# Kernel optimization log

Measured on AMD Instinct MI355X. Metric: run time of the kernel, lower is better.

Reference implementation:

```python
import jax, jax.numpy as jnp
import numpy as np

B, S = 16, 8192
D_MODEL = 128          # config.moe_intermediate_size
D_HID = 512            # config.intermediate_size
N_EXPERTS = 8
BEH_DIM = 32           # config.behavior_embedding_dim
N_BEH = 16             # config.num_behavior -> embedding rows = N_BEH + 1


def setup_inputs() -> dict:
    key = jax.random.key(0)
    k1, k2, k3, k4, k5, k6 = jax.random.split(key, 6)
    hidden_states = jax.random.normal(k1, (B, S, D_MODEL), dtype=jnp.float32)
    position_index = jax.random.randint(k2, (B, S), 0, N_EXPERTS, dtype=jnp.int32)
    behavior_index = jax.random.randint(k3, (B, S), 0, N_BEH + 1, dtype=jnp.int32)
    din = D_MODEL + BEH_DIM
    # expert weights: wi maps (D_MODEL+BEH_DIM)->D_HID, wo maps D_HID->D_MODEL (no bias)
    Wi = jax.random.normal(k4, (N_EXPERTS, din, D_HID), dtype=jnp.float32) * (din ** -0.5)
    Wo = jax.random.normal(k5, (N_EXPERTS, D_HID, D_MODEL), dtype=jnp.float32) * (D_HID ** -0.5)
    emb = jax.random.normal(k6, (N_BEH + 1, BEH_DIM), dtype=jnp.float32)
    return {"hidden_states": hidden_states, "position_index": position_index,
            "behavior_index": behavior_index, "Wi": Wi, "Wo": Wo, "emb": emb}


def reference(hidden_states, position_index, behavior_index, Wi, Wo, emb):
    # behavior injection: concat learned behavior embedding onto each token
    x = jnp.concatenate([hidden_states, emb[behavior_index]], axis=-1)  # [B,S,Din]
    out = jnp.zeros_like(hidden_states)
    # sparse expert dispatch: each token routed to exactly one expert by position_index
    # (loop over small fixed expert count; dropout is identity at p=0 / eval)
    for e in range(Wi.shape[0]):
        h = jax.nn.relu(jnp.einsum('bsd,dh->bsh', x, Wi[e]))   # [B,S,H]
        y = jnp.einsum('bsh,hd->bsd', h, Wo[e])                # [B,S,D]
        out = out + jnp.where((position_index == e)[..., None], y, 0.0)
    return out
```

## Files before the change

### kernel.cpp

```cpp
#include <hip/hip_runtime.h>
#include <stdint.h>

typedef short bf16x8 __attribute__((ext_vector_type(8)));
typedef float f32x4 __attribute__((ext_vector_type(4)));
typedef unsigned short ushort_t;
typedef ushort_t ushort8 __attribute__((ext_vector_type(8)));

#define TOKENS 131072
#define DMODEL 128
#define DIN 160
#define DHID 512
#define NEXP 8
#define BEH 32
#define CAP 24576
#define MT 128
#define TILES (CAP / MT)

#define OFF_COUNTS 0
#define OFF_LISTS  1024
#define OFF_WIP    (OFF_LISTS + NEXP*CAP*4)
#define OFF_WOP    (OFF_WIP + 8*32*5*64*8*2)

#define SCATTER_BLOCKS (TOKENS / 256)
#define NWI (8*32*5*64)
#define NWO (8*8*16*64)
#define PACK_BLOCKS ((NWI + NWO + 255) / 256)

#define STEP_SHORTS 9216

typedef const __attribute__((address_space(1))) uint32_t* gu32p;
typedef __attribute__((address_space(3))) uint32_t* lu32p;

__device__ __forceinline__ ushort_t f2b(float f) {
    union { float f; uint32_t u; } x; x.f = f;
    uint32_t r = x.u + 0x7FFF + ((x.u >> 16) & 1);
    return (ushort_t)(r >> 16);
}

__device__ __forceinline__ uint32_t pk2(float lo, float hi) {
    uint32_t a = __float_as_uint(lo) + 0x8000u;
    uint32_t b = __float_as_uint(hi) + 0x8000u;
    return (a >> 16) | (b & 0xFFFF0000u);
}

__global__ __launch_bounds__(256) void prep_kernel(
    const int* __restrict__ pos, int* __restrict__ counts, int* __restrict__ lists,
    const float* __restrict__ Wi, const float* __restrict__ Wo,
    ushort_t* __restrict__ wiP, ushort_t* __restrict__ woP)
{
    __shared__ int lcnt[NEXP];
    __shared__ int lbase[NEXP];
    int tid = threadIdx.x;
    if (blockIdx.x < SCATTER_BLOCKS) {
        if (tid < NEXP) lcnt[tid] = 0;
        __syncthreads();
        int t = blockIdx.x * 256 + tid;
        int e = pos[t];
        int slot = atomicAdd(&lcnt[e], 1);
        __syncthreads();
        if (tid < NEXP) lbase[tid] = atomicAdd(&counts[tid], lcnt[tid]);
        __syncthreads();
        int p = lbase[e] + slot;
        if (p < CAP) lists[e * CAP + p] = t;
        return;
    }
    int idx = (blockIdx.x - SCATTER_BLOCKS) * 256 + tid;
    if (idx < NWI) {
        int L = idx & 63; int r = idx >> 6;
        int s = r % 5; r /= 5;
        int t1 = r & 31; int e = r >> 5;
        int i = L & 15;
        int u = t1 & 1, sI = t1 >> 1;
        int n = sI * 32 + (i >> 2) * 8 + u * 4 + (i & 3);
        int kb = s * 32 + ((L >> 4) & 3) * 8;
        ushort8 o;
        #pragma unroll
        for (int j = 0; j < 8; ++j)
            o[j] = f2b(Wi[((size_t)e * DIN + kb + j) * DHID + n]);
        *(ushort8*)(wiP + (size_t)idx * 8) = o;
    } else {
        int i2 = idx - NWI;
        if (i2 >= NWO) return;
        int L = i2 & 63; int r = i2 >> 6;
        int ks = r & 15; r >>= 4;
        int t2 = r & 7; int e = r >> 3;
        int n = t2 * 16 + (L & 15);
        int kb = ks * 32 + ((L >> 4) & 3) * 8;
        ushort8 o;
        #pragma unroll
        for (int j = 0; j < 8; ++j)
            o[j] = f2b(Wo[((size_t)e * DHID + kb + j) * DMODEL + n]);
        *(ushort8*)(woP + (size_t)i2 * 8) = o;
    }
}

__device__ __forceinline__ void stage_step(
    const ushort_t* __restrict__ wiPe, const ushort_t* __restrict__ woPe,
    ushort_t* dstBuf, int step, int tid)
{
    #pragma unroll
    for (int it = 0; it < 5; ++it) {
        int g = it * 256 + tid;
        if (it == 4 && tid >= 128) break;
        const ushort_t* src;
        if (g < 640) {
            src = wiPe + (size_t)step * 5120 + (size_t)g * 8;
        } else {
            int g2 = g - 640;
            src = woPe + ((size_t)(((g2 >> 6) * 16 + step) * 64 + (g2 & 63))) * 8;
        }
        __builtin_amdgcn_global_load_lds((gu32p)(const void*)src,
                                         (lu32p)(void*)(dstBuf + g * 8), 16, 0, 0);
    }
}

__device__ __forceinline__ bf16x8 load_x8(const float* __restrict__ hidden,
                                          const float* __restrict__ emb,
                                          int t, int bi, int c0) {
    if (t < 0) return (bf16x8)0;
    const float* src = (c0 < DMODEL) ? (hidden + (size_t)t * DMODEL + c0)
                                     : (emb + (size_t)bi * BEH + (c0 - DMODEL));
    f32x4 p0 = *(const f32x4*)src;
    f32x4 p1 = *(const f32x4*)(src + 4);
    uint32_t d0 = pk2(p0[0], p0[1]), d1 = pk2(p0[2], p0[3]);
    uint32_t d2 = pk2(p1[0], p1[1]), d3 = pk2(p1[2], p1[3]);
    return __builtin_bit_cast(bf16x8, (uint4){d0, d1, d2, d3});
}

__global__ __launch_bounds__(256, 3) void expert_gemm(
    const float* __restrict__ hidden, const int* __restrict__ bindex,
    const int* __restrict__ lists, const int* __restrict__ counts,
    const ushort_t* __restrict__ wiP, const ushort_t* __restrict__ woP,
    const float* __restrict__ emb, float* __restrict__ out)
{
    int e = blockIdx.y;
    int tile = blockIdx.x;
    int count = counts[e]; if (count > CAP) count = CAP;
    int base = tile * MT;
    if (base >= count) return;
    int mvalid = count - base; if (mvalid > MT) mvalid = MT;

    __shared__ ushort_t wbuf[2][STEP_SHORTS];

    int tid = threadIdx.x;
    int lane = tid & 63;
    int w = tid >> 6;
    int l15 = lane & 15;
    int quad = lane >> 4;

    const int* listE = lists + (size_t)e * CAP + base;
    const ushort_t* wiPe = wiP + (size_t)e * 32 * 5 * 64 * 8;
    const ushort_t* woPe = woP + (size_t)e * 8 * 16 * 64 * 8;

    stage_step(wiPe, woPe, wbuf[0], 0, tid);

    bf16x8 xf[2][5];
    int tok[2], bi[2];
    #pragma unroll
    for (int tt = 0; tt < 2; ++tt) {
        int row = w * 32 + tt * 16 + l15;
        tok[tt] = -1; bi[tt] = 0;
        if (row < mvalid) { tok[tt] = listE[row]; bi[tt] = bindex[tok[tt]]; }
    }
    #pragma unroll
    for (int s = 0; s < 5; ++s) {
        int c0 = s * 32 + quad * 8;
        xf[0][s] = load_x8(hidden, emb, tok[0], bi[0], c0);
        xf[1][s] = load_x8(hidden, emb, tok[1], bi[1], c0);
    }

    f32x4 yacc[2][8] = {};

    #pragma unroll 2
    for (int step = 0; step < 16; ++step) {
        int cur = step & 1;
        __syncthreads();
        if (step + 1 < 16)
            stage_step(wiPe, woPe, wbuf[cur ^ 1], step + 1, tid);

        const ushort_t* wiS = wbuf[cur];
        const ushort_t* woS = wbuf[cur] + 5120;

        f32x4 hacc[2][2] = {};
        #pragma unroll
        for (int s = 0; s < 5; ++s) {
            bf16x8 a0 = *(const bf16x8*)&wiS[(0 * 5 + s) * 512 + lane * 8];
            bf16x8 a1 = *(const bf16x8*)&wiS[(1 * 5 + s) * 512 + lane * 8];
            #pragma unroll
            for (int tt = 0; tt < 2; ++tt) {
                hacc[0][tt] = __builtin_amdgcn_mfma_f32_16x16x32_bf16(a0, xf[tt][s], hacc[0][tt], 0, 0, 0);
                hacc[1][tt] = __builtin_amdgcn_mfma_f32_16x16x32_bf16(a1, xf[tt][s], hacc[1][tt], 0, 0, 0);
            }
        }
        bf16x8 afrag[2];
        #pragma unroll
        for (int tt = 0; tt < 2; ++tt) {
            f32x4 h0 = hacc[0][tt], h1 = hacc[1][tt];
            #pragma unroll
            for (int r = 0; r < 4; ++r) {
                h0[r] = h0[r] > 0.f ? h0[r] : 0.f;
                h1[r] = h1[r] > 0.f ? h1[r] : 0.f;
            }
            uint4 dv = { pk2(h0[0], h0[1]), pk2(h0[2], h0[3]),
                         pk2(h1[0], h1[1]), pk2(h1[2], h1[3]) };
            afrag[tt] = __builtin_bit_cast(bf16x8, dv);
        }
        #pragma unroll
        for (int n = 0; n < 8; ++n) {
            bf16x8 b = *(const bf16x8*)&woS[(n * 64 + lane) * 8];
            yacc[0][n] = __builtin_amdgcn_mfma_f32_16x16x32_bf16(afrag[0], b, yacc[0][n], 0, 0, 0);
            yacc[1][n] = __builtin_amdgcn_mfma_f32_16x16x32_bf16(afrag[1], b, yacc[1][n], 0, 0, 0);
        }
    }

    #pragma unroll
    for (int tt = 0; tt < 2; ++tt)
        #pragma unroll
        for (int r = 0; r < 4; ++r) {
            int row = w * 32 + tt * 16 + quad * 4 + r;
            if (row < mvalid) {
                int t = listE[row];
                float* dst = out + (size_t)t * DMODEL + l15;
                #pragma unroll
                for (int n = 0; n < 8; ++n)
                    dst[n * 16] = yacc[tt][n][r];
            }
        }
}

extern "C" void kernel_launch(void* const* d_in, const int* in_sizes, int n_in,
                              void* d_out, int out_size, void* d_ws, size_t ws_size,
                              hipStream_t stream) {
    const float* hidden = (const float*)d_in[0];
    const int*   pos    = (const int*)d_in[1];
    const int*   beh    = (const int*)d_in[2];
    const float* Wi     = (const float*)d_in[3];
    const float* Wo     = (const float*)d_in[4];
    const float* emb    = (const float*)d_in[5];

    char* ws = (char*)d_ws;
    int* counts   = (int*)(ws + OFF_COUNTS);
    int* lists    = (int*)(ws + OFF_LISTS);
    ushort_t* wiP = (ushort_t*)(ws + OFF_WIP);
    ushort_t* woP = (ushort_t*)(ws + OFF_WOP);

    hipMemsetAsync(counts, 0, NEXP * sizeof(int), stream);
    prep_kernel<<<SCATTER_BLOCKS + PACK_BLOCKS, 256, 0, stream>>>(pos, counts, lists, Wi, Wo, wiP, woP);
    expert_gemm<<<dim3(TILES, NEXP), 256, 0, stream>>>(
        hidden, beh, lists, counts, wiP, woP, emb, (float*)d_out);
}
```

Before: 80.82 us.

## Shrink expert GEMM to single-wave 32-row tiles and read Wo from global

Each block of the expert GEMM now holds one wavefront handling 32 tokens instead of four wavefronts handling 128. Only the Wi slice is staged into LDS per step, halving the staging footprint. Wo fragments are loaded straight from global memory into registers each step. This gives four times as many blocks and less LDS per block, which may help occupancy and load balance. The cost is that each block re-reads the full weight set for fewer tokens, so weight traffic through L2 rises and the direct Wo loads are not double-buffered.

```diff
diff --git a/kernel.cpp b/kernel.cpp
--- a/kernel.cpp
+++ b/kernel.cpp
@@ -13,7 +13,7 @@
 #define NEXP 8
 #define BEH 32
 #define CAP 24576
-#define MT 128
+#define MT 32
 #define TILES (CAP / MT)
 
 #define OFF_COUNTS 0
@@ -26,7 +26,7 @@
 #define NWO (8*8*16*64)
 #define PACK_BLOCKS ((NWI + NWO + 255) / 256)
 
-#define STEP_SHORTS 9216
+#define WI_STEP_SHORTS 5120
 
 typedef const __attribute__((address_space(1))) uint32_t* gu32p;
 typedef __attribute__((address_space(3))) uint32_t* lu32p;
@@ -94,21 +94,13 @@
     }
 }
 
-__device__ __forceinline__ void stage_step(
-    const ushort_t* __restrict__ wiPe, const ushort_t* __restrict__ woPe,
-    ushort_t* dstBuf, int step, int tid)
+__device__ __forceinline__ void stage_wi(
+    const ushort_t* __restrict__ wiPe, ushort_t* dstBuf, int step, int lane)
 {
     #pragma unroll
-    for (int it = 0; it < 5; ++it) {
-        int g = it * 256 + tid;
-        if (it == 4 && tid >= 128) break;
-        const ushort_t* src;
-        if (g < 640) {
-            src = wiPe + (size_t)step * 5120 + (size_t)g * 8;
-        } else {
-            int g2 = g - 640;
-            src = woPe + ((size_t)(((g2 >> 6) * 16 + step) * 64 + (g2 & 63))) * 8;
-        }
+    for (int it = 0; it < 10; ++it) {
+        int g = it * 64 + lane;
+        const ushort_t* src = wiPe + (size_t)step * 5120 + (size_t)g * 8;
         __builtin_amdgcn_global_load_lds((gu32p)(const void*)src,
                                          (lu32p)(void*)(dstBuf + g * 8), 16, 0, 0);
     }
@@ -127,7 +119,7 @@
     return __builtin_bit_cast(bf16x8, (uint4){d0, d1, d2, d3});
 }
 
-__global__ __launch_bounds__(256, 3) void expert_gemm(
+__global__ __launch_bounds__(64, 2) void expert_gemm(
     const float* __restrict__ hidden, const int* __restrict__ bindex,
     const int* __restrict__ lists, const int* __restrict__ counts,
     const ushort_t* __restrict__ wiP, const ushort_t* __restrict__ woP,
@@ -140,11 +132,9 @@
     if (base >= count) return;
     int mvalid = count - base; if (mvalid > MT) mvalid = MT;
 
-    __shared__ ushort_t wbuf[2][STEP_SHORTS];
-
-    int tid = threadIdx.x;
-    int lane = tid & 63;
-    int w = tid >> 6;
+    __shared__ ushort_t wbuf[2][WI_STEP_SHORTS];
+
+    int lane = threadIdx.x & 63;
     int l15 = lane & 15;
     int quad = lane >> 4;
 
@@ -152,13 +142,13 @@
     const ushort_t* wiPe = wiP + (size_t)e * 32 * 5 * 64 * 8;
     const ushort_t* woPe = woP + (size_t)e * 8 * 16 * 64 * 8;
 
-    stage_step(wiPe, woPe, wbuf[0], 0, tid);
+    stage_wi(wiPe, wbuf[0], 0, lane);
 
     bf16x8 xf[2][5];
     int tok[2], bi[2];
     #pragma unroll
     for (int tt = 0; tt < 2; ++tt) {
-        int row = w * 32 + tt * 16 + l15;
+        int row = tt * 16 + l15;
         tok[tt] = -1; bi[tt] = 0;
         if (row < mvalid) { tok[tt] = listE[row]; bi[tt] = bindex[tok[tt]]; }
     }
@@ -175,11 +165,16 @@
     for (int step = 0; step < 16; ++step) {
         int cur = step & 1;
         __syncthreads();
+
+        bf16x8 wof[8];
+        #pragma unroll
+        for (int n = 0; n < 8; ++n)
+            wof[n] = *(const bf16x8*)&woPe[((size_t)(n * 16 + step) * 64 + lane) * 8];
+
         if (step + 1 < 16)
-            stage_step(wiPe, woPe, wbuf[cur ^ 1], step + 1, tid);
+            stage_wi(wiPe, wbuf[cur ^ 1], step + 1, lane);
 
         const ushort_t* wiS = wbuf[cur];
-        const ushort_t* woS = wbuf[cur] + 5120;
 
         f32x4 hacc[2][2] = {};
         #pragma unroll
@@ -207,9 +202,8 @@
         }
         #pragma unroll
         for (int n = 0; n < 8; ++n) {
-            bf16x8 b = *(const bf16x8*)&woS[(n * 64 + lane) * 8];
-            yacc[0][n] = __builtin_amdgcn_mfma_f32_16x16x32_bf16(afrag[0], b, yacc[0][n], 0, 0, 0);
-            yacc[1][n] = __builtin_amdgcn_mfma_f32_16x16x32_bf16(afrag[1], b, yacc[1][n], 0, 0, 0);
+            yacc[0][n] = __builtin_amdgcn_mfma_f32_16x16x32_bf16(afrag[0], wof[n], yacc[0][n], 0, 0, 0);
+            yacc[1][n] = __builtin_amdgcn_mfma_f32_16x16x32_bf16(afrag[1], wof[n], yacc[1][n], 0, 0, 0);
         }
     }
 
@@ -217,7 +211,7 @@
     for (int tt = 0; tt < 2; ++tt)
         #pragma unroll
         for (int r = 0; r < 4; ++r) {
-            int row = w * 32 + tt * 16 + quad * 4 + r;
+            int row = tt * 16 + quad * 4 + r;
             if (row < mvalid) {
                 int t = listE[row];
                 float* dst = out + (size_t)t * DMODEL + l15;
@@ -246,6 +240,6 @@
 
     hipMemsetAsync(counts, 0, NEXP * sizeof(int), stream);
     prep_kernel<<<SCATTER_BLOCKS + PACK_BLOCKS, 256, 0, stream>>>(pos, counts, lists, Wi, Wo, wiP, woP);
-    expert_gemm<<<dim3(TILES, NEXP), 256, 0, stream>>>(
+    expert_gemm<<<dim3(TILES, NEXP), 64, 0, stream>>>(
         hidden, beh, lists, counts, wiP, woP, emb, (float*)d_out);
 }
```

Result: slower. 91.08 us (+12.7%).
